# Performance work log

Measured on AMD Instinct MI355X. Metric: run time of the kernel, lower is better.

Reference implementation:

```python
import jax, jax.numpy as jnp
import numpy as np

NUM_HEADS = 12
ALPHA = 0.5
TANH_CLIP = 5.0


def setup_inputs() -> dict:
    key = jax.random.key(0)
    k1, k2, k3, k4, k5 = jax.random.split(key, 5)
    B, N, C = 8, 1024, 768
    x = jax.random.normal(k1, (B, N, C), dtype=jnp.float32)
    # qkv: Linear(C -> 3C), proj: Linear(C -> C); torch stores weight as [out, in]
    s = 1.0 / np.sqrt(C)
    qkv_w = jax.random.normal(k2, (3 * C, C), dtype=jnp.float32) * s
    qkv_b = jax.random.normal(k3, (3 * C,), dtype=jnp.float32) * 0.02
    proj_w = jax.random.normal(k4, (C, C), dtype=jnp.float32) * s
    proj_b = jax.random.normal(k5, (C,), dtype=jnp.float32) * 0.02
    return {"x": x, "qkv_w": qkv_w, "qkv_b": qkv_b, "proj_w": proj_w, "proj_b": proj_b}


def reference(x, qkv_w, qkv_b, proj_w, proj_b):
    B, N, C = x.shape
    H = NUM_HEADS
    D = C // H
    scale = D ** -0.5
    # qkv projection -> [B, N, 3, H, D] -> q/k/v each [B, H, N, D]
    qkv = (x @ qkv_w.T + qkv_b).reshape(B, N, 3, H, D)
    qkv = jnp.transpose(qkv, (2, 0, 3, 1, 4))
    q, k, v = qkv[0], qkv[1], qkv[2]
    # pre-softmax scores [B, H, N, N]
    scores = jnp.einsum("bhnd,bhmd->bhnm", q * scale, k)
    scores_t = jnp.swapaxes(scores, -2, -1)
    scores_sym = 0.5 * (scores + scores_t)
    scores_asym = 0.5 * (scores - scores_t)
    scores = scores_sym + ALPHA * scores_asym
    # gamma_mode == 'approx'
    gamma = np.sqrt((1.0 + ALPHA ** 2) / 2.0)
    scores = scores / gamma
    # tanh clip
    scores = TANH_CLIP * jnp.tanh(scores / TANH_CLIP)
    attn = jax.nn.softmax(scores, axis=-1)
    out = jnp.einsum("bhnm,bhmd->bhnd", attn, v)  # [B, H, N, D]
    out = jnp.transpose(out, (0, 2, 1, 3)).reshape(B, N, C)
    return out @ proj_w.T + proj_b
```

## Files before the change

### kernel.cpp

```cpp
#include <hip/hip_runtime.h>
#include <hip/hip_bf16.h>
#include <stdint.h>

typedef unsigned short u16;
typedef __attribute__((ext_vector_type(8))) short bf16x8;
typedef __attribute__((ext_vector_type(4))) float f32x4;

#define LDS_AS(p) ((__attribute__((address_space(3))) void*)(p))
#define GLB_AS(p) ((__attribute__((address_space(1))) void*)(p))

__device__ __forceinline__ u16 f2bf(float f) {
  union { float f; uint32_t u; } v; v.f = f;
  uint32_t u = v.u;
  u += 0x7fffu + ((u >> 16) & 1u);
  return (u16)(u >> 16);
}

__device__ __forceinline__ float exp2_fast(float x) {
  float r;
  asm("v_exp_f32 %0, %1" : "=v"(r) : "v"(x));
  return r;
}

__device__ __forceinline__ uint32_t f2bits(float f) {
  union { float f; uint32_t u; } v; v.f = f; return v.u;
}
__device__ __forceinline__ uint32_t pack_hi16(uint32_t lo_src, uint32_t hi_src) {
  return __builtin_amdgcn_perm(hi_src, lo_src, 0x07060302u);
}

__device__ __forceinline__ void cvt8(const float* __restrict__ s, u16* __restrict__ d) {
  const float4* sv = (const float4*)s;
  float4 a = sv[0], b = sv[1];
  uint4 o;
  o.x = (uint32_t)f2bf(a.x) | ((uint32_t)f2bf(a.y) << 16);
  o.y = (uint32_t)f2bf(a.z) | ((uint32_t)f2bf(a.w) << 16);
  o.z = (uint32_t)f2bf(b.x) | ((uint32_t)f2bf(b.y) << 16);
  o.w = (uint32_t)f2bf(b.z) | ((uint32_t)f2bf(b.w) << 16);
  *(uint4*)d = o;
}

__global__ __launch_bounds__(256) void k_convert(
    const float* __restrict__ x, const float* __restrict__ wq, const float* __restrict__ wp,
    u16* __restrict__ xb, u16* __restrict__ wqb, u16* __restrict__ wpb) {
  int tid = blockIdx.x * 256 + threadIdx.x;
  int np  = gridDim.x * 256;
  for (int i = tid; i < (8192*768)/8; i += np) cvt8(x  + (size_t)i*8, xb  + (size_t)i*8);
  for (int i = tid; i < (2304*768)/8; i += np) cvt8(wq + (size_t)i*8, wqb + (size_t)i*8);
  for (int i = tid; i < (768*768)/8;  i += np) cvt8(wp + (size_t)i*8, wpb + (size_t)i*8);
}

template<bool SWAP>
__device__ __forceinline__ void gemm_core(const u16* __restrict__ A,
                                          const u16* __restrict__ B,
                                          u16* As, u16* Bs,
                                          int rowA0, int rowB0,
                                          f32x4 acc[4][4]) {
  const int t  = threadIdx.x;
  const int lane = t & 63;
  const int wv = t >> 6;
  const int wr = wv >> 1, wc = wv & 1;
  const int lr = lane & 15, lg = lane >> 4;

#define GSTAGE(KT, BUF)                                                                         \
  {                                                                                             \
    _Pragma("unroll")                                                                           \
    for (int p = 0; p < 2; ++p) {                                                               \
      int idx = p * 256 + t;                                                                    \
      int row = idx >> 2;                                                                       \
      int cc  = (idx & 3) ^ ((row >> 1) & 3);                                                   \
      __builtin_amdgcn_global_load_lds(GLB_AS(A + (size_t)(rowA0 + row) * 768 + (KT) * 32 + cc * 8), \
                                       LDS_AS(As + (BUF) * 4096 + idx * 8), 16, 0, 0);          \
    }                                                                                           \
    _Pragma("unroll")                                                                           \
    for (int p = 0; p < 2; ++p) {                                                               \
      int idx = p * 256 + t;                                                                    \
      int row = idx >> 2;                                                                       \
      int cc  = (idx & 3) ^ ((row >> 1) & 3);                                                   \
      __builtin_amdgcn_global_load_lds(GLB_AS(B + (size_t)(rowB0 + row) * 768 + (KT) * 32 + cc * 8), \
                                       LDS_AS(Bs + (BUF) * 4096 + idx * 8), 16, 0, 0);          \
    }                                                                                           \
  }

  GSTAGE(0, 0);

#pragma unroll 1
  for (int kt = 0; kt < 24; ++kt) {
    const int cur = kt & 1;
    __syncthreads();

    if (kt < 23) GSTAGE(kt + 1, cur ^ 1);

    const u16* Ab = As + cur * 4096;
    const u16* Bb = Bs + cur * 4096;
    bf16x8 af[4], bf_[4];
#pragma unroll
    for (int mi = 0; mi < 4; ++mi) {
      int row = wr * 64 + mi * 16 + lr;
      int cc  = lg ^ ((row >> 1) & 3);
      af[mi] = *(const bf16x8*)(Ab + row * 32 + cc * 8);
    }
#pragma unroll
    for (int ni = 0; ni < 4; ++ni) {
      int row = wc * 64 + ni * 16 + lr;
      int cc  = lg ^ ((row >> 1) & 3);
      bf_[ni] = *(const bf16x8*)(Bb + row * 32 + cc * 8);
    }
#pragma unroll
    for (int mi = 0; mi < 4; ++mi)
#pragma unroll
      for (int ni = 0; ni < 4; ++ni) {
        if (SWAP)
          acc[mi][ni] = __builtin_amdgcn_mfma_f32_16x16x32_bf16(bf_[ni], af[mi], acc[mi][ni], 0, 0, 0);
        else
          acc[mi][ni] = __builtin_amdgcn_mfma_f32_16x16x32_bf16(af[mi], bf_[ni], acc[mi][ni], 0, 0, 0);
      }
  }
#undef GSTAGE
}

__global__ __launch_bounds__(256) void k_gemm_qkv(
    const u16* __restrict__ Aq, const u16* __restrict__ Bw, const float* __restrict__ bias,
    u16* __restrict__ Qh, u16* __restrict__ Kh, u16* __restrict__ Vt) {
  __shared__ u16 As[2 * 128 * 32];
  __shared__ u16 Bs[2 * 128 * 32];
  int bid = blockIdx.x;
  int wg  = (bid & 7) * 144 + (bid >> 3);
  int bx  = wg % 18, by = wg / 18;

  const int t = threadIdx.x, lane = t & 63, wv = t >> 6;
  const int wr = wv >> 1, wc = wv & 1, lr = lane & 15, lg = lane >> 4;
  const int tsec = bx / 6;
  const int colBase = bx * 128 + wc * 64;

  const float gam = 0.7905694150420949f;
  const float rC1 = __builtin_sqrtf(0.57707801636f);
  const float sc1 = __builtin_sqrtf(0.09375f / gam) * rC1;
  const float sc2 = __builtin_sqrtf(0.03125f / gam) * rC1;

  f32x4 acc[4][4];
#pragma unroll
  for (int mi = 0; mi < 4; ++mi)
#pragma unroll
    for (int ni = 0; ni < 4; ++ni) acc[mi][ni] = (f32x4){0.f, 0.f, 0.f, 0.f};

  if (tsec < 2) {
    gemm_core<true>(Aq, Bw, As, Bs, by * 128, bx * 128, acc);

    float4 bv4[4];
#pragma unroll
    for (int ni = 0; ni < 4; ++ni)
      bv4[ni] = *(const float4*)(bias + colBase + ni * 16 + lg * 4);

#pragma unroll
    for (int mi = 0; mi < 4; ++mi) {
      int n = by * 128 + wr * 64 + mi * 16 + lr;
      int b = n >> 10, nn = n & 1023;
#pragma unroll
      for (int ni = 0; ni < 4; ++ni) {
        int fs = colBase - tsec * 768 + ni * 16 + lg * 4;
        int h = fs >> 6, d = fs & 63;
        size_t rowq = ((size_t)(b * 12 + h) * 1024 + nn) * 128;
        float v0 = acc[mi][ni][0] + bv4[ni].x;
        float v1 = acc[mi][ni][1] + bv4[ni].y;
        float v2 = acc[mi][ni][2] + bv4[ni].z;
        float v3 = acc[mi][ni][3] + bv4[ni].w;
        uint2 wq_, wk_;
        wq_.x = (uint32_t)f2bf(v0 * sc1) | ((uint32_t)f2bf(v1 * sc1) << 16);
        wq_.y = (uint32_t)f2bf(v2 * sc1) | ((uint32_t)f2bf(v3 * sc1) << 16);
        wk_.x = (uint32_t)f2bf(v0 * sc2) | ((uint32_t)f2bf(v1 * sc2) << 16);
        wk_.y = (uint32_t)f2bf(v2 * sc2) | ((uint32_t)f2bf(v3 * sc2) << 16);
        if (tsec == 0) {
          *(uint2*)(Qh + rowq + d)      = wq_;
          *(uint2*)(Kh + rowq + 64 + d) = wk_;
        } else {
          *(uint2*)(Kh + rowq + d)      = wq_;
          *(uint2*)(Qh + rowq + 64 + d) = wk_;
        }
      }
    }
  } else {
    gemm_core<false>(Aq, Bw, As, Bs, by * 128, bx * 128, acc);

    float bv[4];
#pragma unroll
    for (int ni = 0; ni < 4; ++ni) bv[ni] = bias[colBase + ni * 16 + lr];

#pragma unroll
    for (int mi = 0; mi < 4; ++mi) {
      int tok0 = by * 128 + wr * 64 + mi * 16 + lg * 4;
      int b = tok0 >> 10, n0 = tok0 & 1023;
#pragma unroll
      for (int ni = 0; ni < 4; ++ni) {
        int fs = colBase - 2 * 768 + ni * 16 + lr;
        int h = fs >> 6, d = fs & 63;
        float v0 = acc[mi][ni][0] + bv[ni];
        float v1 = acc[mi][ni][1] + bv[ni];
        float v2 = acc[mi][ni][2] + bv[ni];
        float v3 = acc[mi][ni][3] + bv[ni];
        uint2 w;
        w.x = (uint32_t)f2bf(v0) | ((uint32_t)f2bf(v1) << 16);
        w.y = (uint32_t)f2bf(v2) | ((uint32_t)f2bf(v3) << 16);
        *(uint2*)(Vt + ((size_t)((b * 12 + h) * 64 + d)) * 1024 + n0) = w;
      }
    }
  }
}

__global__ __launch_bounds__(256, 3) void k_attn(
    const u16* __restrict__ Qh, const u16* __restrict__ Kh, const u16* __restrict__ Vt,
    u16* __restrict__ attn) {
  __shared__ u16 Ks[64 * 128];
  __shared__ u16 Vs[2][64 * 64];
  __shared__ u16 Ps[4][2][32 * 40];

  int bid = blockIdx.x;
  int wg = (bid & 7) * 96 + (bid >> 3);
  int bh = wg >> 3, qb = wg & 7;
  int b = bh / 12, h = bh % 12;

  const int t = threadIdx.x, lane = t & 63, wv = t >> 6;
  const int lr = lane & 15, lg = lane >> 4;

  const size_t khb = (size_t)bh * 1024 * 128;
  const size_t vtb = (size_t)bh * 64 * 1024;

  bf16x8 qf[2][4];
  {
    const u16* qp = Qh + ((size_t)bh * 1024 + qb * 128 + wv * 32 + lr) * 128 + lg * 8;
#pragma unroll
    for (int it = 0; it < 2; ++it)
#pragma unroll
      for (int kk = 0; kk < 4; ++kk)
        qf[it][kk] = *(const bf16x8*)(qp + it * 16 * 128 + kk * 32);
  }

  const short ONE = (short)0x3F80;
  const bf16x8 ones8 = {ONE, ONE, ONE, ONE, ONE, ONE, ONE, ONE};

#define STAGE_K(KT)                                                                            \
  {                                                                                            \
    _Pragma("unroll")                                                                          \
    for (int p = 0; p < 4; ++p) {                                                              \
      int idx = p * 256 + t;                                                                   \
      int row = idx >> 4;                                                                      \
      int cc  = (idx & 15) ^ (row & 7);                                                        \
      __builtin_amdgcn_global_load_lds(GLB_AS(Kh + khb + (size_t)((KT) * 64 + row) * 128 + cc * 8), \
                                       LDS_AS(Ks + idx * 8), 16, 0, 0);                        \
    }                                                                                          \
  }
#define STAGE_V(KT, BUF)                                                                       \
  {                                                                                            \
    _Pragma("unroll")                                                                          \
    for (int p = 0; p < 2; ++p) {                                                              \
      int idx = p * 256 + t;                                                                   \
      int d   = idx >> 3;                                                                      \
      int g   = (idx & 7) ^ (d & 7);                                                           \
      __builtin_amdgcn_global_load_lds(GLB_AS(Vt + vtb + (size_t)d * 1024 + (KT) * 64 + g * 8),\
                                       LDS_AS(Vs[BUF] + idx * 8), 16, 0, 0);                   \
    }                                                                                          \
  }

  STAGE_V(0, 0);
  STAGE_K(0);

  f32x4 acc_o[4][2];
#pragma unroll
  for (int dt = 0; dt < 4; ++dt)
#pragma unroll
    for (int it = 0; it < 2; ++it) acc_o[dt][it] = (f32x4){0.f, 0.f, 0.f, 0.f};
  f32x4 acc_sum[2];
#pragma unroll
  for (int it = 0; it < 2; ++it) acc_sum[it] = (f32x4){0.f, 0.f, 0.f, 0.f};

  const float C2 = -14.4269504089f;

#pragma unroll 1
  for (int kt = 0; kt < 16; ++kt) {
    const int cur = kt & 1;
    __syncthreads();

    if (kt < 15) STAGE_V(kt + 1, cur ^ 1);

    f32x4 accs[4][2];
#pragma unroll
    for (int jt = 0; jt < 4; ++jt)
#pragma unroll
      for (int it = 0; it < 2; ++it) accs[jt][it] = (f32x4){0.f, 0.f, 0.f, 0.f};
    __builtin_amdgcn_s_setprio(1);
#pragma unroll
    for (int jt = 0; jt < 4; ++jt) {
#pragma unroll
      for (int kk = 0; kk < 4; ++kk) {
        int row = jt * 16 + lr;
        int cc  = (kk * 4 + lg) ^ (row & 7);
        bf16x8 kf = *(const bf16x8*)(Ks + row * 128 + cc * 8);
#pragma unroll
        for (int it = 0; it < 2; ++it)
          accs[jt][it] = __builtin_amdgcn_mfma_f32_16x16x32_bf16(kf, qf[it][kk], accs[jt][it], 0, 0, 0);
      }
    }
    __builtin_amdgcn_s_setprio(0);

    __syncthreads();
    if (kt < 15) STAGE_K(kt + 1);

#pragma unroll
    for (int jt = 0; jt < 4; ++jt) {
      const int ks = jt >> 1, jtl = jt & 1;
#pragma unroll
      for (int it = 0; it < 2; ++it) {
        float p0 = exp2_fast(C2 * __builtin_amdgcn_rcpf(exp2_fast(accs[jt][it][0]) + 1.0f));
        float p1 = exp2_fast(C2 * __builtin_amdgcn_rcpf(exp2_fast(accs[jt][it][1]) + 1.0f));
        float p2 = exp2_fast(C2 * __builtin_amdgcn_rcpf(exp2_fast(accs[jt][it][2]) + 1.0f));
        float p3 = exp2_fast(C2 * __builtin_amdgcn_rcpf(exp2_fast(accs[jt][it][3]) + 1.0f));
        uint2 w;
        w.x = pack_hi16(f2bits(p0), f2bits(p1));
        w.y = pack_hi16(f2bits(p2), f2bits(p3));
        *(uint2*)(&Ps[wv][ks][(it * 16 + lr) * 40 + jtl * 16 + lg * 4]) = w;
      }
    }

    asm volatile("" ::: "memory");

    {
      const u16* V0 = Vs[cur];
#pragma unroll
      for (int ks = 0; ks < 2; ++ks) {
        bf16x8 pa[2];
#pragma unroll
        for (int it = 0; it < 2; ++it)
          pa[it] = *(const bf16x8*)(&Ps[wv][ks][(it * 16 + lr) * 40 + lg * 8]);
        __builtin_amdgcn_s_setprio(1);
#pragma unroll
        for (int dt = 0; dt < 4; ++dt) {
          int row  = dt * 16 + lr;
          int slot = (ks * 4 + lg) ^ (lr & 7);
          bf16x8 vf = *(const bf16x8*)(V0 + row * 64 + slot * 8);
#pragma unroll
          for (int it = 0; it < 2; ++it)
            acc_o[dt][it] = __builtin_amdgcn_mfma_f32_16x16x32_bf16(vf, pa[it], acc_o[dt][it], 0, 0, 0);
        }
#pragma unroll
        for (int it = 0; it < 2; ++it)
          acc_sum[it] = __builtin_amdgcn_mfma_f32_16x16x32_bf16(ones8, pa[it], acc_sum[it], 0, 0, 0);
        __builtin_amdgcn_s_setprio(0);
      }
    }
  }
#undef STAGE_K
#undef STAGE_V

  float rinv[2];
#pragma unroll
  for (int it = 0; it < 2; ++it)
    rinv[it] = __builtin_amdgcn_rcpf(acc_sum[it][0]);

#pragma unroll
  for (int dt = 0; dt < 4; ++dt) {
#pragma unroll
    for (int it = 0; it < 2; ++it) {
      float v0 = acc_o[dt][it][0] * rinv[it];
      float v1 = acc_o[dt][it][1] * rinv[it];
      float v2 = acc_o[dt][it][2] * rinv[it];
      float v3 = acc_o[dt][it][3] * rinv[it];
      uint2 w;
      w.x = (uint32_t)f2bf(v0) | ((uint32_t)f2bf(v1) << 16);
      w.y = (uint32_t)f2bf(v2) | ((uint32_t)f2bf(v3) << 16);
      int n = qb * 128 + wv * 32 + it * 16 + lr;
      *(uint2*)(attn + ((size_t)(b * 1024 + n)) * 768 + h * 64 + dt * 16 + lg * 4) = w;
    }
  }
}

__global__ __launch_bounds__(256) void k_gemm_proj(
    const u16* __restrict__ Ain, const u16* __restrict__ Bw, const float* __restrict__ bias,
    float* __restrict__ out) {
  __shared__ u16 As[2 * 128 * 32];
  __shared__ u16 Bs[2 * 128 * 32];
  int bid = blockIdx.x;
  int wg  = (bid & 7) * 48 + (bid >> 3);
  int bx  = wg % 6, by = wg / 6;

  f32x4 acc[4][4];
#pragma unroll
  for (int mi = 0; mi < 4; ++mi)
#pragma unroll
    for (int ni = 0; ni < 4; ++ni) acc[mi][ni] = (f32x4){0.f, 0.f, 0.f, 0.f};

  gemm_core<false>(Ain, Bw, As, Bs, by * 128, bx * 128, acc);

  const int t = threadIdx.x, lane = t & 63, wv = t >> 6;
  const int wr = wv >> 1, wc = wv & 1, lr = lane & 15, lg = lane >> 4;
  const int col0 = bx * 128 + wc * 64;

  float bv[4];
#pragma unroll
  for (int ni = 0; ni < 4; ++ni) bv[ni] = bias[col0 + ni * 16 + lr];

#pragma unroll
  for (int mi = 0; mi < 4; ++mi) {
    int tok0 = by * 128 + wr * 64 + mi * 16 + lg * 4;
#pragma unroll
    for (int ni = 0; ni < 4; ++ni) {
      int col = col0 + ni * 16 + lr;
#pragma unroll
      for (int r = 0; r < 4; ++r) {
        out[(size_t)(tok0 + r) * 768 + col] = acc[mi][ni][r] + bv[ni];
      }
    }
  }
}

extern "C" void kernel_launch(void* const* d_in, const int* in_sizes, int n_in,
                              void* d_out, int out_size, void* d_ws, size_t ws_size,
                              hipStream_t stream) {
  (void)in_sizes; (void)n_in; (void)out_size;
  const float* x      = (const float*)d_in[0];
  const float* qkv_w  = (const float*)d_in[1];
  const float* qkv_b  = (const float*)d_in[2];
  const float* proj_w = (const float*)d_in[3];
  const float* proj_b = (const float*)d_in[4];
  float* out = (float*)d_out;

  uint8_t* ws = (uint8_t*)d_ws;
  u16* xb  = (u16*)(ws + 0);
  u16* wqb = (u16*)(ws + 12582912);
  u16* wpb = (u16*)(ws + 16121856);
  u16* Qh  = (u16*)(ws + 17301504);
  u16* Kh  = (u16*)(ws + 42467328);
  u16* Vt  = (u16*)(ws + 80216064);
  if (ws_size < 92798976) return;

  u16* attnb = xb;

  k_convert<<<2048, 256, 0, stream>>>(x, qkv_w, proj_w, xb, wqb, wpb);
  k_gemm_qkv<<<1152, 256, 0, stream>>>(xb, wqb, qkv_b, Qh, Kh, Vt);
  k_attn<<<768, 256, 0, stream>>>(Qh, Kh, Vt, attnb);
  k_gemm_proj<<<384, 256, 0, stream>>>(attnb, wpb, proj_b, out);
}
```

Baseline: 140.8 us.

## Store Q and K once at width 64 and form the mixed score inside attention

The QKV epilogue now writes a single scaled 64-wide Q and K per head instead of two concatenated 128-wide augmented arrays. The attention kernel stages both K and Q tiles into shared memory and forms the asymmetric score as q·k + k·(q/3) using two MFMA passes with the query-side K held in registers scaled by one third. This halves the global write traffic of the QKV epilogue and keeps the attention MFMA count the same. The cost is extra shared memory for the Q tile, per-element bf16 rescaling in registers, and an extra bf16 rounding of the scaled K that could slightly change numerics.

Measured after the change: 136.6 us. 1.03x faster.

```diff
diff --git a/kernel.cpp b/kernel.cpp
--- a/kernel.cpp
+++ b/kernel.cpp
@@ -22,11 +22,27 @@
   return r;
 }
 
+__device__ __forceinline__ float bits2f(uint32_t u) {
+  union { uint32_t u; float f; } v; v.u = u; return v.f;
+}
 __device__ __forceinline__ uint32_t f2bits(float f) {
   union { float f; uint32_t u; } v; v.f = f; return v.u;
 }
 __device__ __forceinline__ uint32_t pack_hi16(uint32_t lo_src, uint32_t hi_src) {
   return __builtin_amdgcn_perm(hi_src, lo_src, 0x07060302u);
+}
+
+__device__ __forceinline__ bf16x8 scale_third(bf16x8 v) {
+  union { bf16x8 v; uint32_t u[4]; } a, r;
+  a.v = v;
+  const float K = 0.33333333333f;
+#pragma unroll
+  for (int i = 0; i < 4; ++i) {
+    float lo = bits2f(a.u[i] << 16) * K;
+    float hi = bits2f(a.u[i] & 0xFFFF0000u) * K;
+    r.u[i] = pack_hi16(f2bits(lo), f2bits(hi));
+  }
+  return r.v;
 }
 
 __device__ __forceinline__ void cvt8(const float* __restrict__ s, u16* __restrict__ d) {
@@ -136,7 +152,6 @@
   const float gam = 0.7905694150420949f;
   const float rC1 = __builtin_sqrtf(0.57707801636f);
   const float sc1 = __builtin_sqrtf(0.09375f / gam) * rC1;
-  const float sc2 = __builtin_sqrtf(0.03125f / gam) * rC1;
 
   f32x4 acc[4][4];
 #pragma unroll
@@ -146,6 +161,8 @@
 
   if (tsec < 2) {
     gemm_core<true>(Aq, Bw, As, Bs, by * 128, bx * 128, acc);
+
+    u16* dst = (tsec == 0) ? Qh : Kh;
 
     float4 bv4[4];
 #pragma unroll
@@ -160,23 +177,15 @@
       for (int ni = 0; ni < 4; ++ni) {
         int fs = colBase - tsec * 768 + ni * 16 + lg * 4;
         int h = fs >> 6, d = fs & 63;
-        size_t rowq = ((size_t)(b * 12 + h) * 1024 + nn) * 128;
-        float v0 = acc[mi][ni][0] + bv4[ni].x;
-        float v1 = acc[mi][ni][1] + bv4[ni].y;
-        float v2 = acc[mi][ni][2] + bv4[ni].z;
-        float v3 = acc[mi][ni][3] + bv4[ni].w;
-        uint2 wq_, wk_;
-        wq_.x = (uint32_t)f2bf(v0 * sc1) | ((uint32_t)f2bf(v1 * sc1) << 16);
-        wq_.y = (uint32_t)f2bf(v2 * sc1) | ((uint32_t)f2bf(v3 * sc1) << 16);
-        wk_.x = (uint32_t)f2bf(v0 * sc2) | ((uint32_t)f2bf(v1 * sc2) << 16);
-        wk_.y = (uint32_t)f2bf(v2 * sc2) | ((uint32_t)f2bf(v3 * sc2) << 16);
-        if (tsec == 0) {
-          *(uint2*)(Qh + rowq + d)      = wq_;
-          *(uint2*)(Kh + rowq + 64 + d) = wk_;
-        } else {
-          *(uint2*)(Kh + rowq + d)      = wq_;
-          *(uint2*)(Qh + rowq + 64 + d) = wk_;
-        }
+        size_t rowq = ((size_t)(b * 12 + h) * 1024 + nn) * 64;
+        float v0 = (acc[mi][ni][0] + bv4[ni].x) * sc1;
+        float v1 = (acc[mi][ni][1] + bv4[ni].y) * sc1;
+        float v2 = (acc[mi][ni][2] + bv4[ni].z) * sc1;
+        float v3 = (acc[mi][ni][3] + bv4[ni].w) * sc1;
+        uint2 w;
+        w.x = (uint32_t)f2bf(v0) | ((uint32_t)f2bf(v1) << 16);
+        w.y = (uint32_t)f2bf(v2) | ((uint32_t)f2bf(v3) << 16);
+        *(uint2*)(dst + rowq + d) = w;
       }
     }
   } else {
@@ -210,7 +219,8 @@
 __global__ __launch_bounds__(256, 3) void k_attn(
     const u16* __restrict__ Qh, const u16* __restrict__ Kh, const u16* __restrict__ Vt,
     u16* __restrict__ attn) {
-  __shared__ u16 Ks[64 * 128];
+  __shared__ u16 Ks[64 * 64];
+  __shared__ u16 Qs[64 * 64];
   __shared__ u16 Vs[2][64 * 64];
   __shared__ u16 Ps[4][2][32 * 40];
 
@@ -222,31 +232,42 @@
   const int t = threadIdx.x, lane = t & 63, wv = t >> 6;
   const int lr = lane & 15, lg = lane >> 4;
 
-  const size_t khb = (size_t)bh * 1024 * 128;
+  const size_t khb = (size_t)bh * 1024 * 64;
   const size_t vtb = (size_t)bh * 64 * 1024;
 
-  bf16x8 qf[2][4];
+  bf16x8 qf[2][2], kreg[2][2];
   {
-    const u16* qp = Qh + ((size_t)bh * 1024 + qb * 128 + wv * 32 + lr) * 128 + lg * 8;
+    const u16* qp = Qh + ((size_t)bh * 1024 + qb * 128 + wv * 32 + lr) * 64 + lg * 8;
+    const u16* kp = Kh + ((size_t)bh * 1024 + qb * 128 + wv * 32 + lr) * 64 + lg * 8;
 #pragma unroll
     for (int it = 0; it < 2; ++it)
 #pragma unroll
-      for (int kk = 0; kk < 4; ++kk)
-        qf[it][kk] = *(const bf16x8*)(qp + it * 16 * 128 + kk * 32);
+      for (int kk = 0; kk < 2; ++kk) {
+        qf[it][kk]   = *(const bf16x8*)(qp + it * 16 * 64 + kk * 32);
+        kreg[it][kk] = scale_third(*(const bf16x8*)(kp + it * 16 * 64 + kk * 32));
+      }
   }
 
   const short ONE = (short)0x3F80;
   const bf16x8 ones8 = {ONE, ONE, ONE, ONE, ONE, ONE, ONE, ONE};
 
-#define STAGE_K(KT)                                                                            \
+#define STAGE_KQ(KT)                                                                           \
   {                                                                                            \
     _Pragma("unroll")                                                                          \
-    for (int p = 0; p < 4; ++p) {                                                              \
+    for (int p = 0; p < 2; ++p) {                                                              \
       int idx = p * 256 + t;                                                                   \
-      int row = idx >> 4;                                                                      \
-      int cc  = (idx & 15) ^ (row & 7);                                                        \
-      __builtin_amdgcn_global_load_lds(GLB_AS(Kh + khb + (size_t)((KT) * 64 + row) * 128 + cc * 8), \
+      int row = idx >> 3;                                                                      \
+      int g   = (idx & 7) ^ (row & 7);                                                         \
+      __builtin_amdgcn_global_load_lds(GLB_AS(Kh + khb + (size_t)((KT) * 64 + row) * 64 + g * 8), \
                                        LDS_AS(Ks + idx * 8), 16, 0, 0);                        \
+    }                                                                                          \
+    _Pragma("unroll")                                                                          \
+    for (int p = 0; p < 2; ++p) {                                                              \
+      int idx = p * 256 + t;                                                                   \
+      int row = idx >> 3;                                                                      \
+      int g   = (idx & 7) ^ (row & 7);                                                         \
+      __builtin_amdgcn_global_load_lds(GLB_AS(Qh + khb + (size_t)((KT) * 64 + row) * 64 + g * 8), \
+                                       LDS_AS(Qs + idx * 8), 16, 0, 0);                        \
     }                                                                                          \
   }
 #define STAGE_V(KT, BUF)                                                                       \
@@ -262,7 +283,7 @@
   }
 
   STAGE_V(0, 0);
-  STAGE_K(0);
+  STAGE_KQ(0);
 
   f32x4 acc_o[4][2];
 #pragma unroll
@@ -290,20 +311,28 @@
     __builtin_amdgcn_s_setprio(1);
 #pragma unroll
     for (int jt = 0; jt < 4; ++jt) {
-#pragma unroll
-      for (int kk = 0; kk < 4; ++kk) {
-        int row = jt * 16 + lr;
-        int cc  = (kk * 4 + lg) ^ (row & 7);
-        bf16x8 kf = *(const bf16x8*)(Ks + row * 128 + cc * 8);
+      int row = jt * 16 + lr;
+#pragma unroll
+      for (int kk = 0; kk < 2; ++kk) {
+        int cc = (kk * 4 + lg) ^ (row & 7);
+        bf16x8 kf = *(const bf16x8*)(Ks + row * 64 + cc * 8);
 #pragma unroll
         for (int it = 0; it < 2; ++it)
           accs[jt][it] = __builtin_amdgcn_mfma_f32_16x16x32_bf16(kf, qf[it][kk], accs[jt][it], 0, 0, 0);
       }
+#pragma unroll
+      for (int kk = 0; kk < 2; ++kk) {
+        int cc = (kk * 4 + lg) ^ (row & 7);
+        bf16x8 qsf = *(const bf16x8*)(Qs + row * 64 + cc * 8);
+#pragma unroll
+        for (int it = 0; it < 2; ++it)
+          accs[jt][it] = __builtin_amdgcn_mfma_f32_16x16x32_bf16(qsf, kreg[it][kk], accs[jt][it], 0, 0, 0);
+      }
     }
     __builtin_amdgcn_s_setprio(0);
 
     __syncthreads();
-    if (kt < 15) STAGE_K(kt + 1);
+    if (kt < 15) STAGE_KQ(kt + 1);
 
 #pragma unroll
     for (int jt = 0; jt < 4; ++jt) {
@@ -348,7 +377,7 @@
       }
     }
   }
-#undef STAGE_K
+#undef STAGE_KQ
 #undef STAGE_V
 
   float rinv[2];
```
